# Kernel tuning notes

Hardware: AMD Instinct MI355X
Metric: run time of the kernel (lower is better)

The kernel has to match this reference:

```python
import jax, jax.numpy as jnp
import numpy as np

EPS = 1e-6  # torch F.pairwise_distance eps, added to the difference elementwise

B, Z = 8192, 128
N_CLASSES = 62
P = int(N_CLASSES * 1.5)  # 93 proxies


def pdist(a, b):
    """||a_i - b_j + EPS||_2 for all pairs, without a [N,M,Z] intermediate.
    Expansion: ||a-b||^2 + 2*EPS*sum(a-b) + Z*EPS^2."""
    aa = jnp.sum(a * a, axis=-1)[:, None]
    bb = jnp.sum(b * b, axis=-1)[None, :]
    ab = a @ b.T
    eps_term = 2.0 * EPS * (jnp.sum(a, -1)[:, None] - jnp.sum(b, -1)[None, :]) + a.shape[-1] * EPS * EPS
    return jnp.sqrt(jnp.maximum(aa + bb - 2.0 * ab + eps_term, 0.0))


def setup_inputs() -> dict:
    key = jax.random.key(0)
    k0, k1, k2 = jax.random.split(key, 3)
    z = jax.random.normal(k0, (B, Z), dtype=jnp.float32)
    y_idx = jax.random.randint(k1, (B,), 0, N_CLASSES, dtype=jnp.int32)
    proxies = jax.random.uniform(k2, (P, Z), dtype=jnp.float32)  # nn.init.uniform_
    y_map = jnp.arange(N_CLASSES, dtype=jnp.int32)  # y_to_relative_y_train (unique classes)
    return {"z": z, "y_idx": y_idx, "proxies": proxies, "y_map": y_map}


def reference(z, y_idx, proxies, y_map):
    # F.normalize(proxies, p=2, dim=-1) with 1e-12 clamp
    prx = proxies / jnp.maximum(jnp.linalg.norm(proxies, axis=-1, keepdims=True), 1e-12)
    # y_rel[j] = position where y_to_relative_y_train == y_idx[j] (exactly one match)
    y_rel = jnp.argmax(y_map[None, :] == y_idx[:, None], axis=-1)  # [B]

    anchors = np.arange(0, z.shape[0] - 3, 3)  # static anchor indices i
    z_a = z[anchors]                            # [A,Z]

    # nearest proxy to each anchor
    D_prox = pdist(z_a, prx)                    # [A,P]
    prox_p = prx[jnp.argmin(D_prox, axis=-1)]   # [A,Z]

    # distance from chosen proxy to every sample; restrict to suffix j>=i with same class
    D_pz = pdist(prox_p, z)                     # [A,B]
    mask = (np.arange(z.shape[0])[None, :] >= anchors[:, None]) & \
           (y_rel[None, :] == y_rel[anchors][:, None])  # [A,B], row i always has j=i True
    D_pos = jnp.where(mask, D_pz, -jnp.inf)
    j_p = jnp.argmax(D_pos, axis=-1)            # hardest positive index
    D_p = jnp.take_along_axis(D_pos, j_p[:, None], axis=-1)[:, 0]  # [A]

    # distances from hardest positive to all proxies -> NCA denominator
    D_n = pdist(z[j_p], prx)                    # [A,P]
    losses = D_p + jax.nn.logsumexp(-D_n, axis=-1)  # -log(exp(-D_p)/sum exp(-D_n))
    return jnp.mean(losses)
```

## Files before the change

kernel.cpp:

```cpp
#include <hip/hip_runtime.h>
#include <math.h>

#define B_N   8192
#define Z_D   128
#define P_N   93
#define NCLS  62
#define A_N   2730
#define BCAP  256
#define GT_S  96
#define NPART 683
#define TWO_EPS   2e-6f
#define ZEPS2     (128.0f * 1e-6f * 1e-6f)

#define AT_LD(p)      __hip_atomic_load((p), __ATOMIC_RELAXED, __HIP_MEMORY_SCOPE_AGENT)
#define AT_ST(p, v)   __hip_atomic_store((p), (v), __ATOMIC_RELAXED, __HIP_MEMORY_SCOPE_AGENT)
#define AT_ADDU(p, v) __hip_atomic_fetch_add((p), (v), __ATOMIC_RELAXED, __HIP_MEMORY_SCOPE_AGENT)

__device__ __forceinline__ float wave_sum(float v) {
#pragma unroll
  for (int off = 1; off < 64; off <<= 1) v += __shfl_xor(v, off, 64);
  return v;
}
__device__ __forceinline__ float wave_min(float v) {
#pragma unroll
  for (int off = 1; off < 64; off <<= 1) v = fminf(v, __shfl_xor(v, off, 64));
  return v;
}

__global__ __launch_bounds__(512) void kA(
    const float* __restrict__ z, const int* __restrict__ y_idx,
    const float* __restrict__ prox, const int* __restrict__ y_map,
    float* __restrict__ pp, float* __restrict__ sp,
    float* __restrict__ zz, float* __restrict__ sz, float* __restrict__ w,
    int* __restrict__ cnt, int* __restrict__ bkt, float* __restrict__ GT,
    unsigned int* __restrict__ ctr) {
  __shared__ float linv[6];
  __shared__ float pt[6 * Z_D];
  __shared__ int lcnt;
  const int b = blockIdx.x, tid = threadIdx.x;
  const int lane = tid & 63, wv = tid >> 6;

  if (b == 0 && tid < 17) ctr[tid * 32] = 0u;

  if (b < 256) {
    const int jch = b & 15, kt = b >> 4, k0 = kt * 6;
    const int nk = (kt == 15) ? 3 : 6;
    const int j = jch * 512 + tid;
    const float* __restrict__ zrow = z + (size_t)j * Z_D;
    if (wv < nk) {
      const int k = k0 + wv;
      const float a = prox[k * Z_D + lane];
      const float c = prox[k * Z_D + 64 + lane];
      const float s = wave_sum(a + c);
      const float q = wave_sum(a * a + c * c);
      const float inv = 1.0f / fmaxf(sqrtf(q), 1e-12f);
      if (lane == 0) {
        linv[wv] = inv;
        if (jch == 0) { pp[k] = q * inv * inv; sp[k] = s * inv; }
      }
    }
    __syncthreads();
    {
      const int nf = nk * 32;
      const float4* __restrict__ src = (const float4*)(prox + (size_t)k0 * Z_D);
      for (int t = tid; t < nf; t += 512) {
        const float iv = linv[t >> 5];
        const float4 v = src[t];
        ((float4*)pt)[t] = make_float4(v.x * iv, v.y * iv, v.z * iv, v.w * iv);
      }
    }
    __syncthreads();
    if (kt < 15) {
      float a0 = 0, a1 = 0, a2 = 0, a3 = 0, a4 = 0, a5 = 0;
#pragma unroll 8
      for (int i4 = 0; i4 < Z_D; i4 += 4) {
        const float4 zv = *(const float4*)(zrow + i4);
        const int f = i4 >> 2;
        const float4 q0 = ((const float4*)pt)[0 * 32 + f];
        const float4 q1 = ((const float4*)pt)[1 * 32 + f];
        const float4 q2 = ((const float4*)pt)[2 * 32 + f];
        const float4 q3 = ((const float4*)pt)[3 * 32 + f];
        const float4 q4 = ((const float4*)pt)[4 * 32 + f];
        const float4 q5 = ((const float4*)pt)[5 * 32 + f];
        a0 += zv.x * q0.x + zv.y * q0.y + zv.z * q0.z + zv.w * q0.w;
        a1 += zv.x * q1.x + zv.y * q1.y + zv.z * q1.z + zv.w * q1.w;
        a2 += zv.x * q2.x + zv.y * q2.y + zv.z * q2.z + zv.w * q2.w;
        a3 += zv.x * q3.x + zv.y * q3.y + zv.z * q3.z + zv.w * q3.w;
        a4 += zv.x * q4.x + zv.y * q4.y + zv.z * q4.z + zv.w * q4.w;
        a5 += zv.x * q5.x + zv.y * q5.y + zv.z * q5.z + zv.w * q5.w;
      }
      float* g = GT + (size_t)j * GT_S + k0;
      *(float2*)(g + 0) = make_float2(a0, a1);
      *(float2*)(g + 2) = make_float2(a2, a3);
      *(float2*)(g + 4) = make_float2(a4, a5);
    } else {
      float a0 = 0, a1 = 0, a2 = 0, zs = 0, zq = 0;
#pragma unroll 8
      for (int i4 = 0; i4 < Z_D; i4 += 4) {
        const float4 zv = *(const float4*)(zrow + i4);
        const int f = i4 >> 2;
        const float4 q0 = ((const float4*)pt)[0 * 32 + f];
        const float4 q1 = ((const float4*)pt)[1 * 32 + f];
        const float4 q2 = ((const float4*)pt)[2 * 32 + f];
        zs += zv.x + zv.y + zv.z + zv.w;
        zq += zv.x * zv.x + zv.y * zv.y + zv.z * zv.z + zv.w * zv.w;
        a0 += zv.x * q0.x + zv.y * q0.y + zv.z * q0.z + zv.w * q0.w;
        a1 += zv.x * q1.x + zv.y * q1.y + zv.z * q1.z + zv.w * q1.w;
        a2 += zv.x * q2.x + zv.y * q2.y + zv.z * q2.z + zv.w * q2.w;
      }
      float* g = GT + (size_t)j * GT_S + 90;
      *(float2*)(g) = make_float2(a0, a1);
      g[2] = a2;
      zz[j] = zq;
      sz[j] = zs;
      w[j] = zq - TWO_EPS * zs;
    }
  } else {
    const int c = b - 256;
    if (tid == 0) lcnt = 0;
    __syncthreads();
    const int ym = y_map[c];
    for (int j = tid; j < B_N; j += 512) {
      if (y_idx[j] == ym) {
        const int pos = atomicAdd(&lcnt, 1);
        if (pos < BCAP) bkt[c * BCAP + pos] = j;
      }
    }
    __syncthreads();
    if (tid == 0) cnt[c] = min(lcnt, BCAP);
  }
}

__global__ __launch_bounds__(256) void kB2(
    const int* __restrict__ y_idx, const int* __restrict__ y_map,
    const float* __restrict__ pp, const float* __restrict__ sp,
    const float* __restrict__ zz, const float* __restrict__ sz,
    const float* __restrict__ w,
    const int* __restrict__ cnt, const int* __restrict__ bkt,
    const float* __restrict__ GT, float* partial, unsigned int* ctr,
    float* __restrict__ out) {
  __shared__ float lpp[P_N], lsp[P_N];
  __shared__ int lymap[NCLS];
  __shared__ float part[4];
  const int b = blockIdx.x;
  const int tid = threadIdx.x, lane = tid & 63, wv = tid >> 6;
  if (tid < P_N) { lpp[tid] = pp[tid]; lsp[tid] = sp[tid]; }
  if (tid < NCLS) lymap[tid] = y_map[tid];
  __syncthreads();

  const int wid = b * 4 + wv;
  float loss = 0.0f;
  if (wid < A_N) {
    const int i = 3 * wid;
    const int yi = y_idx[i];
    const unsigned long long mm = __ballot(lane < NCLS && lymap[lane] == yi);
    const int cls = __ffsll(mm) - 1;
    const float zzi = zz[i], szi = sz[i];
    const int kB = lane + 64;

    const float* __restrict__ GTi = GT + (size_t)i * GT_S;
    float v1 = fmaxf(zzi + lpp[lane] - 2.0f * GTi[lane] +
                     TWO_EPS * (szi - lsp[lane]) + ZEPS2, 0.0f);
    int i1 = lane;
    if (kB < P_N) {
      const float v2 = fmaxf(zzi + lpp[kB] - 2.0f * GTi[kB] +
                             TWO_EPS * (szi - lsp[kB]) + ZEPS2, 0.0f);
      if (v2 < v1) { v1 = v2; i1 = kB; }
    }
#pragma unroll
    for (int off = 1; off < 64; off <<= 1) {
      const float ov = __shfl_xor(v1, off, 64);
      const int oi = __shfl_xor(i1, off, 64);
      if (ov < v1 || (ov == v1 && oi < i1)) { v1 = ov; i1 = oi; }
    }
    const int p = i1;

    const float cp = lpp[p] + TWO_EPS * lsp[p] + ZEPS2;
    const int n = cnt[cls];
    const int* __restrict__ bk = bkt + cls * BCAP;
    float best = -INFINITY;
    int bestj = 0x7fffffff;
    for (int t = lane; t < n; t += 64) {
      const int jj = bk[t];
      if (jj >= i) {
        const float vv = fmaxf(cp + w[jj] - 2.0f * GT[(size_t)jj * GT_S + p], 0.0f);
        if (vv > best || (vv == best && jj < bestj)) { best = vv; bestj = jj; }
      }
    }
#pragma unroll
    for (int off = 1; off < 64; off <<= 1) {
      const float ov = __shfl_xor(best, off, 64);
      const int oj = __shfl_xor(bestj, off, 64);
      if (ov > best || (ov == best && oj < bestj)) { best = ov; bestj = oj; }
    }
    const float Dp = sqrtf(best);
    const int jp = bestj;

    const float zzj = zz[jp], szj = sz[jp];
    const float* __restrict__ GTj = GT + (size_t)jp * GT_S;
    const float d1 = sqrtf(fmaxf(zzj + lpp[lane] - 2.0f * GTj[lane] +
                                 TWO_EPS * (szj - lsp[lane]) + ZEPS2, 0.0f));
    float d2 = INFINITY;
    if (kB < P_N)
      d2 = sqrtf(fmaxf(zzj + lpp[kB] - 2.0f * GTj[kB] +
                       TWO_EPS * (szj - lsp[kB]) + ZEPS2, 0.0f));
    const float mn = wave_min(fminf(d1, d2));
    float ss = expf(mn - d1) + ((kB < P_N) ? expf(mn - d2) : 0.0f);
    ss = wave_sum(ss);
    loss = Dp - mn + logf(ss);
  }
  if (lane == 0) part[wv] = (wid < A_N) ? loss : 0.0f;
  __syncthreads();

  if (wv == 0) {
    int last = 0;
    if (lane == 0) {
      AT_ST(&partial[b], part[0] + part[1] + part[2] + part[3]);
      __builtin_amdgcn_s_waitcnt(0);
      const int sub = b & 15;
      const unsigned quota = (sub < 11) ? 43u : 42u;
      const unsigned old = AT_ADDU(&ctr[sub * 32], 1u);
      if (old == quota - 1u) {
        const unsigned so = AT_ADDU(&ctr[16 * 32], 1u);
        if (so == 15u) last = 1;
      }
    }
    last = __shfl(last, 0, 64);
    if (last) {
      float s = 0.0f;
#pragma unroll
      for (int r = 0; r < 11; ++r) {
        const int t = lane + r * 64;
        if (t < NPART) s += AT_LD(&partial[t]);
      }
      s = wave_sum(s);
      if (lane == 0) out[0] = s * (1.0f / (float)A_N);
    }
  }
}

extern "C" void kernel_launch(void* const* d_in, const int* in_sizes, int n_in,
                              void* d_out, int out_size, void* d_ws, size_t ws_size,
                              hipStream_t stream) {
  const float* z = (const float*)d_in[0];
  const int* y_idx = (const int*)d_in[1];
  const float* prox = (const float*)d_in[2];
  const int* y_map = (const int*)d_in[3];
  float* out = (float*)d_out;

  char* ws = (char*)d_ws;
  unsigned int* ctr = (unsigned int*)(ws + 0);
  float* pp    = (float*)(ws + 2560);
  float* sp    = (float*)(ws + 3072);
  float* zz    = (float*)(ws + 3584);
  float* sz    = (float*)(ws + 36352);
  float* w     = (float*)(ws + 69120);
  int*   cnt   = (int*)  (ws + 101888);
  int*   bkt   = (int*)  (ws + 102144);
  float* parts = (float*)(ws + 165632);
  float* GT    = (float*)(ws + 168448);

  kA<<<256 + NCLS, 512, 0, stream>>>(z, y_idx, prox, y_map,
                                     pp, sp, zz, sz, w, cnt, bkt, GT, ctr);
  kB2<<<NPART, 256, 0, stream>>>(y_idx, y_map, pp, sp, zz, sz, w,
                                 cnt, bkt, GT, parts, ctr, out);
}
```

Baseline: 81.44 us.

## Split each anchor's positive search across two waves with unrolled bucket loads

Each anchor is now handled by a pair of waves instead of one. Each wave scans half of the class bucket (up to 256 entries, two per lane) with loads issued up front rather than in a strided loop, and the two partial maxima are merged through shared memory. The block count doubles, the final-reduction quota and loop are adjusted, and the GT workspace offset moves to make room for more partials. This adds a block-level sync and duplicates the nearest-proxy work in both waves. It also drops the bound on the bucket count, so it always reads all BCAP entries.

Result: no change. 82.22 us (+1.0%).

```diff
diff --git a/kernel.cpp b/kernel.cpp
--- a/kernel.cpp
+++ b/kernel.cpp
@@ -8,7 +8,7 @@
 #define A_N   2730
 #define BCAP  256
 #define GT_S  96
-#define NPART 683
+#define NPART 1365
 #define TWO_EPS   2e-6f
 #define ZEPS2     (128.0f * 1e-6f * 1e-6f)
 
@@ -141,60 +141,75 @@
     float* __restrict__ out) {
   __shared__ float lpp[P_N], lsp[P_N];
   __shared__ int lymap[NCLS];
-  __shared__ float part[4];
+  __shared__ float bw_v[4];
+  __shared__ int bw_j[4];
+  __shared__ float part[2];
   const int b = blockIdx.x;
   const int tid = threadIdx.x, lane = tid & 63, wv = tid >> 6;
+  const int pair = wv >> 1, half = wv & 1;
   if (tid < P_N) { lpp[tid] = pp[tid]; lsp[tid] = sp[tid]; }
   if (tid < NCLS) lymap[tid] = y_map[tid];
   __syncthreads();
 
-  const int wid = b * 4 + wv;
-  float loss = 0.0f;
-  if (wid < A_N) {
-    const int i = 3 * wid;
-    const int yi = y_idx[i];
-    const unsigned long long mm = __ballot(lane < NCLS && lymap[lane] == yi);
-    const int cls = __ffsll(mm) - 1;
-    const float zzi = zz[i], szi = sz[i];
-    const int kB = lane + 64;
-
-    const float* __restrict__ GTi = GT + (size_t)i * GT_S;
-    float v1 = fmaxf(zzi + lpp[lane] - 2.0f * GTi[lane] +
-                     TWO_EPS * (szi - lsp[lane]) + ZEPS2, 0.0f);
-    int i1 = lane;
-    if (kB < P_N) {
-      const float v2 = fmaxf(zzi + lpp[kB] - 2.0f * GTi[kB] +
-                             TWO_EPS * (szi - lsp[kB]) + ZEPS2, 0.0f);
-      if (v2 < v1) { v1 = v2; i1 = kB; }
-    }
-#pragma unroll
-    for (int off = 1; off < 64; off <<= 1) {
-      const float ov = __shfl_xor(v1, off, 64);
-      const int oi = __shfl_xor(i1, off, 64);
-      if (ov < v1 || (ov == v1 && oi < i1)) { v1 = ov; i1 = oi; }
-    }
-    const int p = i1;
-
-    const float cp = lpp[p] + TWO_EPS * lsp[p] + ZEPS2;
-    const int n = cnt[cls];
-    const int* __restrict__ bk = bkt + cls * BCAP;
-    float best = -INFINITY;
-    int bestj = 0x7fffffff;
-    for (int t = lane; t < n; t += 64) {
-      const int jj = bk[t];
-      if (jj >= i) {
-        const float vv = fmaxf(cp + w[jj] - 2.0f * GT[(size_t)jj * GT_S + p], 0.0f);
-        if (vv > best || (vv == best && jj < bestj)) { best = vv; bestj = jj; }
-      }
-    }
-#pragma unroll
-    for (int off = 1; off < 64; off <<= 1) {
-      const float ov = __shfl_xor(best, off, 64);
-      const int oj = __shfl_xor(bestj, off, 64);
-      if (ov > best || (ov == best && oj < bestj)) { best = ov; bestj = oj; }
-    }
-    const float Dp = sqrtf(best);
-    const int jp = bestj;
+  const int wid = b * 2 + pair;
+  const int i = 3 * wid;
+  const int yi = y_idx[i];
+  const unsigned long long mm = __ballot(lane < NCLS && lymap[lane] == yi);
+  const int cls = __ffsll(mm) - 1;
+  const int* __restrict__ bk = bkt + cls * BCAP;
+
+  const int n = cnt[cls];
+  const int t0 = half * 64 + lane, t1 = t0 + 128;
+  const int e0 = bk[t0], e1 = bk[t1];
+  const float zzi = zz[i], szi = sz[i];
+  const int kB = lane + 64;
+
+  const float* __restrict__ GTi = GT + (size_t)i * GT_S;
+  float v1 = fmaxf(zzi + lpp[lane] - 2.0f * GTi[lane] +
+                   TWO_EPS * (szi - lsp[lane]) + ZEPS2, 0.0f);
+  int i1 = lane;
+  if (kB < P_N) {
+    const float v2 = fmaxf(zzi + lpp[kB] - 2.0f * GTi[kB] +
+                           TWO_EPS * (szi - lsp[kB]) + ZEPS2, 0.0f);
+    if (v2 < v1) { v1 = v2; i1 = kB; }
+  }
+#pragma unroll
+  for (int off = 1; off < 64; off <<= 1) {
+    const float ov = __shfl_xor(v1, off, 64);
+    const int oi = __shfl_xor(i1, off, 64);
+    if (ov < v1 || (ov == v1 && oi < i1)) { v1 = ov; i1 = oi; }
+  }
+  const int p = i1;
+
+  const float cp = lpp[p] + TWO_EPS * lsp[p] + ZEPS2;
+  const bool a0ok = (t0 < n) && (e0 >= i);
+  const bool a1ok = (t1 < n) && (e1 >= i);
+  const int r0 = a0ok ? e0 : i;
+  const int r1 = a1ok ? e1 : i;
+  const float w0 = w[r0], g0 = GT[(size_t)r0 * GT_S + p];
+  const float w1 = w[r1], g1 = GT[(size_t)r1 * GT_S + p];
+  float best = -INFINITY;
+  int bestj = 0x7fffffff;
+  if (a0ok) { best = fmaxf(cp + w0 - 2.0f * g0, 0.0f); bestj = e0; }
+  if (a1ok) {
+    const float vv = fmaxf(cp + w1 - 2.0f * g1, 0.0f);
+    if (vv > best || (vv == best && e1 < bestj)) { best = vv; bestj = e1; }
+  }
+#pragma unroll
+  for (int off = 1; off < 64; off <<= 1) {
+    const float ov = __shfl_xor(best, off, 64);
+    const int oj = __shfl_xor(bestj, off, 64);
+    if (ov > best || (ov == best && oj < bestj)) { best = ov; bestj = oj; }
+  }
+  if (lane == 0) { bw_v[wv] = best; bw_j[wv] = bestj; }
+  __syncthreads();
+
+  if (half == 0) {
+    float bA = bw_v[wv], bB = bw_v[wv + 1];
+    int jA = bw_j[wv], jB = bw_j[wv + 1];
+    if (bB > bA || (bB == bA && jB < jA)) { bA = bB; jA = jB; }
+    const float Dp = sqrtf(bA);
+    const int jp = jA;
 
     const float zzj = zz[jp], szj = sz[jp];
     const float* __restrict__ GTj = GT + (size_t)jp * GT_S;
@@ -207,18 +222,17 @@
     const float mn = wave_min(fminf(d1, d2));
     float ss = expf(mn - d1) + ((kB < P_N) ? expf(mn - d2) : 0.0f);
     ss = wave_sum(ss);
-    loss = Dp - mn + logf(ss);
-  }
-  if (lane == 0) part[wv] = (wid < A_N) ? loss : 0.0f;
+    if (lane == 0) part[pair] = Dp - mn + logf(ss);
+  }
   __syncthreads();
 
   if (wv == 0) {
     int last = 0;
     if (lane == 0) {
-      AT_ST(&partial[b], part[0] + part[1] + part[2] + part[3]);
+      AT_ST(&partial[b], part[0] + part[1]);
       __builtin_amdgcn_s_waitcnt(0);
       const int sub = b & 15;
-      const unsigned quota = (sub < 11) ? 43u : 42u;
+      const unsigned quota = (sub < 5) ? 86u : 85u;
       const unsigned old = AT_ADDU(&ctr[sub * 32], 1u);
       if (old == quota - 1u) {
         const unsigned so = AT_ADDU(&ctr[16 * 32], 1u);
@@ -228,8 +242,7 @@
     last = __shfl(last, 0, 64);
     if (last) {
       float s = 0.0f;
-#pragma unroll
-      for (int r = 0; r < 11; ++r) {
+      for (int r = 0; r < 22; ++r) {
         const int t = lane + r * 64;
         if (t < NPART) s += AT_LD(&partial[t]);
       }
@@ -258,7 +271,7 @@
   int*   cnt   = (int*)  (ws + 101888);
   int*   bkt   = (int*)  (ws + 102144);
   float* parts = (float*)(ws + 165632);
-  float* GT    = (float*)(ws + 168448);
+  float* GT    = (float*)(ws + 171136);
 
   kA<<<256 + NCLS, 512, 0, stream>>>(z, y_idx, prox, y_map,
                                      pp, sp, zz, sz, w, cnt, bkt, GT, ctr);
```

## Compute z-proxy dot products with bf16 MFMA in a separate kernel

Applied to the files above, without the earlier changes.

Replaces the scalar fp32 z·proxy dot-product kernel with a prep kernel that converts z and the normalized proxies to bf16, plus a new kGT kernel that computes the [B,96] Gram matrix with 16x16x32 bf16 MFMA instructions. Row norms and sums stay in fp32 and are computed in the prep pass. The aim is to move the GEMM onto matrix cores. In exchange it adds a kernel launch, an extra bf16 round trip through memory, and bf16 rounding error that could flip argmin/argmax decisions on near-tied distances.

Result: slower. 89.82 us (+10.3%).

```diff
diff --git a/kernel.cpp b/kernel.cpp
--- a/kernel.cpp
+++ b/kernel.cpp
@@ -16,6 +16,9 @@
 #define AT_ST(p, v)   __hip_atomic_store((p), (v), __ATOMIC_RELAXED, __HIP_MEMORY_SCOPE_AGENT)
 #define AT_ADDU(p, v) __hip_atomic_fetch_add((p), (v), __ATOMIC_RELAXED, __HIP_MEMORY_SCOPE_AGENT)
 
+typedef short bf16x8 __attribute__((ext_vector_type(8)));
+typedef float f32x4 __attribute__((ext_vector_type(4)));
+
 __device__ __forceinline__ float wave_sum(float v) {
 #pragma unroll
   for (int off = 1; off < 64; off <<= 1) v += __shfl_xor(v, off, 64);
@@ -26,108 +29,106 @@
   for (int off = 1; off < 64; off <<= 1) v = fminf(v, __shfl_xor(v, off, 64));
   return v;
 }
-
-__global__ __launch_bounds__(512) void kA(
+__device__ __forceinline__ unsigned short f2bf(float f) {
+  const unsigned u = __float_as_uint(f);
+  return (unsigned short)((u + 0x7FFFu + ((u >> 16) & 1u)) >> 16);
+}
+__device__ __forceinline__ unsigned pk2(float lo, float hi) {
+  return (unsigned)f2bf(lo) | ((unsigned)f2bf(hi) << 16);
+}
+
+__global__ __launch_bounds__(256) void kPrep(
     const float* __restrict__ z, const int* __restrict__ y_idx,
     const float* __restrict__ prox, const int* __restrict__ y_map,
+    unsigned short* __restrict__ zb, unsigned short* __restrict__ pb,
     float* __restrict__ pp, float* __restrict__ sp,
     float* __restrict__ zz, float* __restrict__ sz, float* __restrict__ w,
-    int* __restrict__ cnt, int* __restrict__ bkt, float* __restrict__ GT,
+    int* __restrict__ cnt, int* __restrict__ bkt,
     unsigned int* __restrict__ ctr) {
-  __shared__ float linv[6];
-  __shared__ float pt[6 * Z_D];
   __shared__ int lcnt;
   const int b = blockIdx.x, tid = threadIdx.x;
   const int lane = tid & 63, wv = tid >> 6;
 
-  if (b == 0 && tid < 17) ctr[tid * 32] = 0u;
-
   if (b < 256) {
-    const int jch = b & 15, kt = b >> 4, k0 = kt * 6;
-    const int nk = (kt == 15) ? 3 : 6;
-    const int j = jch * 512 + tid;
-    const float* __restrict__ zrow = z + (size_t)j * Z_D;
-    if (wv < nk) {
-      const int k = k0 + wv;
+    const int row = b * 32 + (tid >> 3);
+    const int p8 = tid & 7;
+    const float* __restrict__ src = z + (size_t)row * Z_D + p8 * 16;
+    const float4 v0 = *(const float4*)(src + 0);
+    const float4 v1 = *(const float4*)(src + 4);
+    const float4 v2 = *(const float4*)(src + 8);
+    const float4 v3 = *(const float4*)(src + 12);
+    float s = v0.x + v0.y + v0.z + v0.w + v1.x + v1.y + v1.z + v1.w +
+              v2.x + v2.y + v2.z + v2.w + v3.x + v3.y + v3.z + v3.w;
+    float q = v0.x*v0.x + v0.y*v0.y + v0.z*v0.z + v0.w*v0.w +
+              v1.x*v1.x + v1.y*v1.y + v1.z*v1.z + v1.w*v1.w +
+              v2.x*v2.x + v2.y*v2.y + v2.z*v2.z + v2.w*v2.w +
+              v3.x*v3.x + v3.y*v3.y + v3.z*v3.z + v3.w*v3.w;
+    uint4 pa, pbv;
+    pa.x = pk2(v0.x, v0.y); pa.y = pk2(v0.z, v0.w);
+    pa.z = pk2(v1.x, v1.y); pa.w = pk2(v1.z, v1.w);
+    pbv.x = pk2(v2.x, v2.y); pbv.y = pk2(v2.z, v2.w);
+    pbv.z = pk2(v3.x, v3.y); pbv.w = pk2(v3.z, v3.w);
+    uint4* dst = (uint4*)(zb + (size_t)row * Z_D + p8 * 16);
+    dst[0] = pa; dst[1] = pbv;
+#pragma unroll
+    for (int off = 1; off < 8; off <<= 1) {
+      s += __shfl_xor(s, off, 64);
+      q += __shfl_xor(q, off, 64);
+    }
+    if (p8 == 0) { zz[row] = q; sz[row] = s; w[row] = q - TWO_EPS * s; }
+  } else if (b < 256 + NCLS) {
+    const int c = b - 256;
+    if (tid == 0) lcnt = 0;
+    __syncthreads();
+    const int ym = y_map[c];
+    for (int j = tid; j < B_N; j += 256) {
+      if (y_idx[j] == ym) {
+        const int pos = atomicAdd(&lcnt, 1);
+        if (pos < BCAP) bkt[c * BCAP + pos] = j;
+      }
+    }
+    __syncthreads();
+    if (tid == 0) cnt[c] = min(lcnt, BCAP);
+  } else {
+    for (int k = wv; k < P_N; k += 4) {
       const float a = prox[k * Z_D + lane];
       const float c = prox[k * Z_D + 64 + lane];
       const float s = wave_sum(a + c);
       const float q = wave_sum(a * a + c * c);
       const float inv = 1.0f / fmaxf(sqrtf(q), 1e-12f);
-      if (lane == 0) {
-        linv[wv] = inv;
-        if (jch == 0) { pp[k] = q * inv * inv; sp[k] = s * inv; }
-      }
-    }
-    __syncthreads();
-    {
-      const int nf = nk * 32;
-      const float4* __restrict__ src = (const float4*)(prox + (size_t)k0 * Z_D);
-      for (int t = tid; t < nf; t += 512) {
-        const float iv = linv[t >> 5];
-        const float4 v = src[t];
-        ((float4*)pt)[t] = make_float4(v.x * iv, v.y * iv, v.z * iv, v.w * iv);
-      }
-    }
-    __syncthreads();
-    if (kt < 15) {
-      float a0 = 0, a1 = 0, a2 = 0, a3 = 0, a4 = 0, a5 = 0;
-#pragma unroll 8
-      for (int i4 = 0; i4 < Z_D; i4 += 4) {
-        const float4 zv = *(const float4*)(zrow + i4);
-        const int f = i4 >> 2;
-        const float4 q0 = ((const float4*)pt)[0 * 32 + f];
-        const float4 q1 = ((const float4*)pt)[1 * 32 + f];
-        const float4 q2 = ((const float4*)pt)[2 * 32 + f];
-        const float4 q3 = ((const float4*)pt)[3 * 32 + f];
-        const float4 q4 = ((const float4*)pt)[4 * 32 + f];
-        const float4 q5 = ((const float4*)pt)[5 * 32 + f];
-        a0 += zv.x * q0.x + zv.y * q0.y + zv.z * q0.z + zv.w * q0.w;
-        a1 += zv.x * q1.x + zv.y * q1.y + zv.z * q1.z + zv.w * q1.w;
-        a2 += zv.x * q2.x + zv.y * q2.y + zv.z * q2.z + zv.w * q2.w;
-        a3 += zv.x * q3.x + zv.y * q3.y + zv.z * q3.z + zv.w * q3.w;
-        a4 += zv.x * q4.x + zv.y * q4.y + zv.z * q4.z + zv.w * q4.w;
-        a5 += zv.x * q5.x + zv.y * q5.y + zv.z * q5.z + zv.w * q5.w;
-      }
-      float* g = GT + (size_t)j * GT_S + k0;
-      *(float2*)(g + 0) = make_float2(a0, a1);
-      *(float2*)(g + 2) = make_float2(a2, a3);
-      *(float2*)(g + 4) = make_float2(a4, a5);
-    } else {
-      float a0 = 0, a1 = 0, a2 = 0, zs = 0, zq = 0;
-#pragma unroll 8
-      for (int i4 = 0; i4 < Z_D; i4 += 4) {
-        const float4 zv = *(const float4*)(zrow + i4);
-        const int f = i4 >> 2;
-        const float4 q0 = ((const float4*)pt)[0 * 32 + f];
-        const float4 q1 = ((const float4*)pt)[1 * 32 + f];
-        const float4 q2 = ((const float4*)pt)[2 * 32 + f];
-        zs += zv.x + zv.y + zv.z + zv.w;
-        zq += zv.x * zv.x + zv.y * zv.y + zv.z * zv.z + zv.w * zv.w;
-        a0 += zv.x * q0.x + zv.y * q0.y + zv.z * q0.z + zv.w * q0.w;
-        a1 += zv.x * q1.x + zv.y * q1.y + zv.z * q1.z + zv.w * q1.w;
-        a2 += zv.x * q2.x + zv.y * q2.y + zv.z * q2.z + zv.w * q2.w;
-      }
-      float* g = GT + (size_t)j * GT_S + 90;
-      *(float2*)(g) = make_float2(a0, a1);
-      g[2] = a2;
-      zz[j] = zq;
-      sz[j] = zs;
-      w[j] = zq - TWO_EPS * zs;
-    }
-  } else {
-    const int c = b - 256;
-    if (tid == 0) lcnt = 0;
-    __syncthreads();
-    const int ym = y_map[c];
-    for (int j = tid; j < B_N; j += 512) {
-      if (y_idx[j] == ym) {
-        const int pos = atomicAdd(&lcnt, 1);
-        if (pos < BCAP) bkt[c * BCAP + pos] = j;
-      }
-    }
-    __syncthreads();
-    if (tid == 0) cnt[c] = min(lcnt, BCAP);
+      pb[k * Z_D + lane] = f2bf(a * inv);
+      pb[k * Z_D + 64 + lane] = f2bf(c * inv);
+      if (lane == 0) { pp[k] = q * inv * inv; sp[k] = s * inv; }
+    }
+    if (wv == 0)
+      for (int t = lane; t < 3 * Z_D; t += 64) pb[P_N * Z_D + t] = 0;
+    if (tid < 17) ctr[tid * 32] = 0u;
+  }
+}
+
+__global__ __launch_bounds__(64) void kGT(
+    const unsigned short* __restrict__ zb, const unsigned short* __restrict__ pb,
+    float* __restrict__ GT) {
+  const int lane = threadIdx.x & 63;
+  const int m = lane & 15, quad = lane >> 4;
+  const int j0 = blockIdx.x * 16;
+  const unsigned short* __restrict__ zrow = zb + (size_t)(j0 + m) * Z_D;
+  bf16x8 af[4];
+#pragma unroll
+  for (int kb = 0; kb < 4; ++kb)
+    af[kb] = *(const bf16x8*)(zrow + kb * 32 + quad * 8);
+#pragma unroll
+  for (int nt = 0; nt < 6; ++nt) {
+    const unsigned short* __restrict__ prow = pb + (size_t)(nt * 16 + m) * Z_D;
+    f32x4 acc = {0.0f, 0.0f, 0.0f, 0.0f};
+#pragma unroll
+    for (int kb = 0; kb < 4; ++kb) {
+      const bf16x8 bfr = *(const bf16x8*)(prow + kb * 32 + quad * 8);
+      acc = __builtin_amdgcn_mfma_f32_16x16x32_bf16(af[kb], bfr, acc, 0, 0, 0);
+    }
+#pragma unroll
+    for (int r = 0; r < 4; ++r)
+      GT[(size_t)(j0 + quad * 4 + r) * GT_S + nt * 16 + m] = acc[r];
   }
 }
 
@@ -259,9 +260,12 @@
   int*   bkt   = (int*)  (ws + 102144);
   float* parts = (float*)(ws + 165632);
   float* GT    = (float*)(ws + 168448);
-
-  kA<<<256 + NCLS, 512, 0, stream>>>(z, y_idx, prox, y_map,
-                                     pp, sp, zz, sz, w, cnt, bkt, GT, ctr);
+  unsigned short* zb = (unsigned short*)(ws + 3314176);
+  unsigned short* pb = (unsigned short*)(ws + 5411328);
+
+  kPrep<<<256 + NCLS + 1, 256, 0, stream>>>(z, y_idx, prox, y_map, zb, pb,
+                                            pp, sp, zz, sz, w, cnt, bkt, ctr);
+  kGT<<<B_N / 16, 64, 0, stream>>>(zb, pb, GT);
   kB2<<<NPART, 256, 0, stream>>>(y_idx, y_map, pp, sp, zz, sz, w,
                                  cnt, bkt, GT, parts, ctr, out);
 }
```
